# Optimization experiments

Measured on AMD Instinct MI355X. Metric: run time of the kernel, lower is better.

The kernel has to match this reference:

```python
import jax, jax.numpy as jnp
import numpy as np

N, E, B, P = 50000, 800000, 64, 3
F_E = F_N = F_G = 16
D, H = 64, 128  # embedding/target dim, hidden dim
NEG_SLOPE = 0.01


def _lrelu(z):
    return jax.nn.leaky_relu(z, NEG_SLOPE)


def _mlp3(z, w1, b1, w2, b2, w3, b3):
    z = _lrelu(z @ w1 + b1)
    z = _lrelu(z @ w2 + b2)
    return z @ w3 + b3


def setup_inputs() -> dict:
    key = jax.random.key(0)
    ks = iter(jax.random.split(key, 64))
    s = 0.05

    def lin(i, o, stack=None):
        shp = (i, o) if stack is None else (stack, i, o)
        return jax.random.normal(next(ks), shp, jnp.float32) * s

    def bias(o, stack=None):
        shp = (o,) if stack is None else (stack, o)
        return jax.random.normal(next(ks), shp, jnp.float32) * s

    inp = {}
    inp['x'] = jax.random.normal(next(ks), (N, F_N), jnp.float32)
    inp['edge_attr'] = jax.random.normal(next(ks), (E, F_E), jnp.float32)
    inp['u'] = jax.random.normal(next(ks), (B, F_G), jnp.float32)
    # embeddings
    inp['emb_e_w'], inp['emb_e_b'] = lin(F_E, D), bias(D)
    inp['emb_n_w'], inp['emb_n_b'] = lin(F_N, D), bias(D)
    inp['emb_g_w'], inp['emb_g_b'] = lin(F_G, D), bias(D)
    # message-passing params, stacked over P passes (dims identical since emb==target)
    inp['ew1'], inp['eb1'] = lin(4 * D, H, P), bias(H, P)   # src,dest,edge,global -> 256
    inp['ew2'], inp['eb2'] = lin(H, H, P), bias(H, P)
    inp['ew3'], inp['eb3'] = lin(H, D, P), bias(D, P)
    inp['nw1'], inp['nb1'] = lin(3 * D, H, P), bias(H, P)   # node,edge_agg,global -> 192
    inp['nw2'], inp['nb2'] = lin(H, H, P), bias(H, P)
    inp['nw3'], inp['nb3'] = lin(H, D, P), bias(D, P)
    inp['gw1'], inp['gb1'] = lin(2 * D, H, P), bias(H, P)   # global,node_agg -> 128
    inp['gw2'], inp['gb2'] = lin(H, H, P), bias(H, P)
    inp['gw3'], inp['gb3'] = lin(H, D, P), bias(D, P)
    # decoders
    inp['dec_w'], inp['dec_b'] = lin(D, 1), bias(1)
    inp['vw1'], inp['vb1'] = lin(D, D), bias(D)
    inp['vw2'], inp['vb2'] = lin(D, 1), bias(1)
    # graph structure
    inp['edge_index'] = jax.random.randint(next(ks), (2, E), 0, N, jnp.int32)
    inp['batch'] = jnp.sort(jax.random.randint(next(ks), (N,), 0, B, jnp.int32))
    return inp


def reference(x, edge_attr, u,
              emb_e_w, emb_e_b, emb_n_w, emb_n_b, emb_g_w, emb_g_b,
              ew1, eb1, ew2, eb2, ew3, eb3,
              nw1, nb1, nw2, nb2, nw3, nb3,
              gw1, gb1, gw2, gb2, gw3, gb3,
              dec_w, dec_b, vw1, vb1, vw2, vb2,
              edge_index, batch):
    n_nodes, n_graphs = x.shape[0], u.shape[0]
    row, col = edge_index[0], edge_index[1]

    # embeddings
    e = _lrelu(edge_attr @ emb_e_w + emb_e_b)   # [E, D]
    xh = _lrelu(x @ emb_n_w + emb_n_b)          # [N, D]
    g = _lrelu(u @ emb_g_w + emb_g_b)           # [B, D]

    for p in range(ew1.shape[0]):
        # EdgeModel: gather src/dest/global, MLP
        e_in = jnp.concatenate([xh[row], xh[col], e, g[batch[row]]], axis=1)
        e_new = _mlp3(e_in, ew1[p], eb1[p], ew2[p], eb2[p], ew3[p], eb3[p])
        # NodeModel: scatter_add NEW edge features to dest nodes
        e_agg = jax.ops.segment_sum(e_new, col, num_segments=n_nodes)
        n_in = jnp.concatenate([xh, e_agg, g[batch]], axis=1)
        x_new = _mlp3(n_in, nw1[p], nb1[p], nw2[p], nb2[p], nw3[p], nb3[p])
        # GlobalModel: scatter_add NEW node features per graph
        x_agg = jax.ops.segment_sum(x_new, batch, num_segments=n_graphs)
        g_in = jnp.concatenate([g, x_agg], axis=1)
        g_new = _mlp3(g_in, gw1[p], gb1[p], gw2[p], gb2[p], gw3[p], gb3[p])
        # residual updates
        xh, e, g = xh + x_new, e + e_new, g + g_new

    edge_out = e @ dec_w + dec_b                      # [E, 1]
    value_out = _lrelu(g @ vw1 + vb1) @ vw2 + vb2     # [B, 1]
    return edge_out, value_out
```

## Files before the change

kernel.cpp:

```cpp
#include <hip/hip_runtime.h>
#include <hip/hip_bf16.h>
#include <stdint.h>

typedef unsigned short u16;
typedef unsigned int u32;
typedef short s16x8 __attribute__((ext_vector_type(8)));
typedef float f32x4 __attribute__((ext_vector_type(4)));

#define NN 50000
#define EE 800000
#define BB 64
#define PP 3

__device__ __forceinline__ float b2f(u16 x){ union{u32 u; float f;} c; c.u=((u32)x)<<16; return c.f; }
__device__ __forceinline__ u16 f2b(float v){ union{float f; u32 u;} c; c.f=v; u32 u=c.u; return (u16)((u + 0x7fffu + ((u>>16)&1u))>>16); }
__device__ __forceinline__ float lrelu(float v){ return v>0.f ? v : 0.01f*v; }
__device__ __forceinline__ f32x4 MFMA(s16x8 a, s16x8 b, f32x4 c){
  return __builtin_amdgcn_mfma_f32_16x16x32_bf16(a,b,c,0,0,0);
}

__device__ __forceinline__ int xcd_swz(int bid, int nwg){
  int q = nwg>>3, r = nwg&7;
  int x = bid&7, i = bid>>3;
  return (x<r ? x*(q+1) : r*(q+1)+(x-r)*q) + i;
}

__global__ __launch_bounds__(256) void k_hist(const int* __restrict__ eidx, int* __restrict__ hist){
  int e = blockIdx.x*256 + threadIdx.x;
  if (e < EE) atomicAdd(&hist[eidx[EE+e]], 1);
}

__global__ __launch_bounds__(1024) void k_scan(const int* __restrict__ hist, int* __restrict__ offs){
  __shared__ int lsums[1024];
  const int tid = threadIdx.x;
  const int CH = 49;
  int base = tid*CH;
  int s = 0;
  for (int i=0;i<CH;i++){ int b=base+i; if (b<NN) s += hist[b]; }
  lsums[tid]=s; __syncthreads();
  for (int off=1; off<1024; off<<=1){
    int v = (tid>=off)? lsums[tid-off] : 0;
    __syncthreads();
    lsums[tid] += v;
    __syncthreads();
  }
  int run = (tid>0)? lsums[tid-1] : 0;
  for (int i=0;i<CH;i++){ int b=base+i; if (b<NN){ offs[b]=run; run+=hist[b]; } }
}

__global__ __launch_bounds__(256) void k_scatter(const int* __restrict__ eidx, int* __restrict__ offs,
                                                 int* __restrict__ perm, int* __restrict__ dcols,
                                                 int* __restrict__ inv){
  int e = blockIdx.x*256 + threadIdx.x;
  if (e >= EE) return;
  int col = eidx[EE+e];
  int pos = atomicAdd(&offs[col], 1);
  perm[pos] = e;
  dcols[pos] = col;
  inv[e] = pos;
}

__global__ __launch_bounds__(256) void k_repack(const float* __restrict__ W, u16* __restrict__ out, int K, int Nn){
  int chunks_pp = (K/32)*(Nn/16)*64;
  int t = blockIdx.x*256 + threadIdx.x;
  if (t >= PP*chunks_pp) return;
  int p = t/chunks_pp, rem = t%chunks_pp;
  int NB = Nn/16;
  int kb = rem/(NB*64); int r2 = rem%(NB*64);
  int nb = r2/64; int l = r2&63;
  const float* Wp = W + (size_t)p*K*Nn;
  int k0 = kb*32 + ((l>>4)<<3), n = nb*16 + (l&15);
  u16 tmp[8];
  #pragma unroll
  for (int j=0;j<8;j++) tmp[j] = f2b(Wp[(size_t)(k0+j)*Nn + n]);
  *(uint4*)(out + (size_t)t*8) = *(uint4*)tmp;
}

template<bool SCATTER>
__global__ __launch_bounds__(256) void k_embed(const float* __restrict__ in, const float* __restrict__ W,
                                               const float* __restrict__ b, u16* __restrict__ out, int nrows,
                                               const int* __restrict__ inv){
  __shared__ float wl[1024];
  __shared__ float bl[64];
  int tid = threadIdx.x;
  for (int i=tid;i<1024;i+=256) wl[i]=W[i];
  if (tid<64) bl[tid]=b[tid];
  __syncthreads();
  int row = blockIdx.x*256 + tid;
  if (row >= nrows) return;
  float inb[16];
  const float4* src4=(const float4*)(in + (size_t)row*16);
  #pragma unroll
  for (int q=0;q<4;q++){ float4 v=src4[q]; inb[q*4]=v.x; inb[q*4+1]=v.y; inb[q*4+2]=v.z; inb[q*4+3]=v.w; }
  float acc[64];
  #pragma unroll
  for (int j=0;j<64;j++) acc[j]=bl[j];
  #pragma unroll
  for (int k=0;k<16;k++){
    float a = inb[k];
    const float4* wr4 = (const float4*)(wl + k*64);
    #pragma unroll
    for (int j4=0;j4<16;j4++){
      float4 w4 = wr4[j4];
      acc[j4*4+0] += a*w4.x; acc[j4*4+1] += a*w4.y;
      acc[j4*4+2] += a*w4.z; acc[j4*4+3] += a*w4.w;
    }
  }
  u16 ob[64];
  #pragma unroll
  for (int j=0;j<64;j++) ob[j]=f2b(lrelu(acc[j]));
  int drow = SCATTER ? inv[row] : row;
  uint4* dst=(uint4*)(out + (size_t)drow*64);
  #pragma unroll
  for (int j=0;j<8;j++) dst[j]=((uint4*)ob)[j];
}

__global__ void k_embed_g(const float* __restrict__ in, const float* __restrict__ W, const float* __restrict__ b,
                          u16* __restrict__ g_b, float* __restrict__ g_f){
  __shared__ float wl[1024];
  __shared__ float bl[64];
  int tid = threadIdx.x;
  for (int i=tid;i<1024;i+=64) wl[i]=W[i];
  if (tid<64) bl[tid]=b[tid];
  __syncthreads();
  int row = tid;
  float inb[16];
  const float4* src4=(const float4*)(in + (size_t)row*16);
  #pragma unroll
  for (int q=0;q<4;q++){ float4 v=src4[q]; inb[q*4]=v.x; inb[q*4+1]=v.y; inb[q*4+2]=v.z; inb[q*4+3]=v.w; }
  float acc[64];
  #pragma unroll
  for (int j=0;j<64;j++) acc[j]=bl[j];
  #pragma unroll
  for (int k=0;k<16;k++){
    float a = inb[k];
    const float* wr = wl + k*64;
    #pragma unroll
    for (int j=0;j<64;j++) acc[j] += a*wr[j];
  }
  #pragma unroll
  for (int j=0;j<64;j++){
    float v = lrelu(acc[j]);
    g_f[row*64+j] = v;
    g_b[row*64+j] = f2b(v);
  }
}

__device__ __forceinline__ void rmw16(u16* p, const float* vals){
  uint4 q0=((uint4*)p)[0], q1=((uint4*)p)[1];
  const u16* h0=(const u16*)&q0; const u16* hq=(const u16*)&q1;
  u16 o[16];
  #pragma unroll
  for (int c=0;c<8;c++) o[c]=f2b(b2f(h0[c])+vals[c]);
  #pragma unroll
  for (int c=0;c<8;c++) o[8+c]=f2b(b2f(hq[c])+vals[8+c]);
  ((uint4*)p)[0]=*(uint4*)o; ((uint4*)p)[1]=*(uint4*)(o+8);
}

template<int K0, int MODE, bool LAST>
__global__ __launch_bounds__(256,4) void k_mlp(
    u16* __restrict__ xh_b, u16* __restrict__ e_b,
    float* __restrict__ eagg, float* __restrict__ xagg,
    u16* __restrict__ g_b, float* __restrict__ g_f,
    const int* __restrict__ eidx, const int* __restrict__ batch,
    const int* __restrict__ perm, const int* __restrict__ dcols,
    const uint4* __restrict__ w1f, const uint4* __restrict__ w2f, const uint4* __restrict__ w3f,
    const float* __restrict__ b1, const float* __restrict__ b2, const float* __restrict__ b3,
    const float* __restrict__ dw, const float* __restrict__ db, float* __restrict__ outp)
{
  constexpr int KB  = K0/32;
  constexpr int RS  = K0*2;
  constexpr int A0SZ = (64*RS > 32768) ? 64*RS : 32768;
  __shared__ __align__(16) char a0[A0SZ];
  __shared__ int s_edge[64];
  __shared__ int s_dcol[64];
  char* h1 = a0;
  char* h2 = a0 + 16384;
  char* h3 = a0;

  const int tid  = threadIdx.x;
  const int wave = tid>>6, lane = tid&63;
  const int rowbase = (MODE==2 ? blockIdx.x : xcd_swz(blockIdx.x, gridDim.x))*64;
  const int lrow = lane&15;
  const int lsw  = (lane&7)<<4;
  const int aoff = (lane>>4)*16;
  const int qc   = (lane>>4)*4;

  s16x8 wA[KB][2];
  #pragma unroll
  for (int kb=0;kb<KB;kb++){
    #pragma unroll
    for (int j=0;j<2;j++)
      wA[kb][j] = *(const s16x8*)(w1f + (size_t)(kb*8 + wave*2 + j)*64 + lane);
  }

  {
    const int r = tid>>2, s = tid&3;
    char* drow = a0 + r*RS;
    const int sw = (r&7)<<4;
    if (MODE==0){
      const int slot = rowbase + r;
      const int edge = perm[slot];
      if (s==0){ s_edge[r]=edge; s_dcol[r]=dcols[slot]; }
      const int er = eidx[edge], ec = eidx[EE+edge];
      const u16* src = (s==0)? xh_b + (size_t)er*64
                     : (s==1)? xh_b + (size_t)ec*64
                     : (s==2)? e_b  + (size_t)slot*64
                     :         g_b  + (size_t)batch[er]*64;
      const uint4* s4=(const uint4*)src;
      #pragma unroll
      for (int j=0;j<8;j++)
        *(uint4*)(drow + ((s*128 + j*16) ^ sw)) = s4[j];
    } else if (MODE==1){
      const int node = rowbase + r;
      const bool ok = node < NN;
      if (s==0){
        const uint4* s4=(const uint4*)(xh_b + (size_t)node*64);
        #pragma unroll
        for (int j=0;j<8;j++){ uint4 v={0,0,0,0}; if (ok) v=s4[j];
          *(uint4*)(drow + ((j*16) ^ sw)) = v; }
      } else if (s==1){
        const float4* s4=(const float4*)(eagg + (size_t)node*64);
        #pragma unroll
        for (int j=0;j<8;j++){
          u16 tmp[8]={0,0,0,0,0,0,0,0};
          if (ok){ float4 lo=s4[2*j], hi=s4[2*j+1];
            tmp[0]=f2b(lo.x);tmp[1]=f2b(lo.y);tmp[2]=f2b(lo.z);tmp[3]=f2b(lo.w);
            tmp[4]=f2b(hi.x);tmp[5]=f2b(hi.y);tmp[6]=f2b(hi.z);tmp[7]=f2b(hi.w); }
          *(uint4*)(drow + ((128 + j*16) ^ sw)) = *(uint4*)tmp;
        }
      } else if (s==2){
        int bidx = ok ? batch[node] : 0;
        const uint4* s4=(const uint4*)(g_b + (size_t)bidx*64);
        #pragma unroll
        for (int j=0;j<8;j++){ uint4 v={0,0,0,0}; if (ok) v=s4[j];
          *(uint4*)(drow + ((256 + j*16) ^ sw)) = v; }
      }
    } else {
      if (s==0){
        const uint4* s4=(const uint4*)(g_b + (size_t)r*64);
        #pragma unroll
        for (int j=0;j<8;j++) *(uint4*)(drow + ((j*16) ^ sw)) = s4[j];
      } else if (s==1){
        const float4* s4=(const float4*)(xagg + (size_t)r*64);
        #pragma unroll
        for (int j=0;j<8;j++){
          u16 tmp[8];
          float4 lo=s4[2*j], hi=s4[2*j+1];
          tmp[0]=f2b(lo.x);tmp[1]=f2b(lo.y);tmp[2]=f2b(lo.z);tmp[3]=f2b(lo.w);
          tmp[4]=f2b(hi.x);tmp[5]=f2b(hi.y);tmp[6]=f2b(hi.z);tmp[7]=f2b(hi.w);
          *(uint4*)(drow + ((128 + j*16) ^ sw)) = *(uint4*)tmp;
        }
      }
    }
  }
  __syncthreads();

  f32x4 acc[4][2];
  #pragma unroll
  for (int rb=0;rb<4;rb++){ acc[rb][0]=f32x4{0,0,0,0}; acc[rb][1]=f32x4{0,0,0,0}; }
  #pragma unroll
  for (int kb=0;kb<KB;kb++){
    #pragma unroll
    for (int rb=0;rb<4;rb++){
      s16x8 af = *(const s16x8*)(a0 + (rb*16+lrow)*RS + ((kb*64 + aoff) ^ lsw));
      acc[rb][0] = MFMA(wA[kb][0], af, acc[rb][0]);
      acc[rb][1] = MFMA(wA[kb][1], af, acc[rb][1]);
    }
  }

  s16x8 wB[4][2];
  #pragma unroll
  for (int kb=0;kb<4;kb++){
    #pragma unroll
    for (int j=0;j<2;j++)
      wB[kb][j] = *(const s16x8*)(w2f + (size_t)(kb*8 + wave*2 + j)*64 + lane);
  }
  __syncthreads();

  #pragma unroll
  for (int j=0;j<2;j++){
    const float4 bs = *(const float4*)(b1 + wave*32 + j*16 + qc);
    #pragma unroll
    for (int rb=0;rb<4;rb++){
      int row = rb*16 + lrow;
      int c2 = (wave*32 + j*16 + qc)*2;
      u16 t0=f2b(lrelu(acc[rb][j][0]+bs.x)), t1=f2b(lrelu(acc[rb][j][1]+bs.y));
      u16 t2=f2b(lrelu(acc[rb][j][2]+bs.z)), t3=f2b(lrelu(acc[rb][j][3]+bs.w));
      uint2 pk = make_uint2((u32)t0 | ((u32)t1<<16), (u32)t2 | ((u32)t3<<16));
      *(uint2*)(h1 + row*256 + (c2 ^ ((row&7)<<4))) = pk;
    }
  }
  __syncthreads();

  f32x4 acc2[4][2];
  #pragma unroll
  for (int rb=0;rb<4;rb++){ acc2[rb][0]=f32x4{0,0,0,0}; acc2[rb][1]=f32x4{0,0,0,0}; }
  #pragma unroll
  for (int kb=0;kb<4;kb++){
    #pragma unroll
    for (int rb=0;rb<4;rb++){
      s16x8 af = *(const s16x8*)(h1 + (rb*16+lrow)*256 + ((kb*64 + aoff) ^ lsw));
      acc2[rb][0] = MFMA(wB[kb][0], af, acc2[rb][0]);
      acc2[rb][1] = MFMA(wB[kb][1], af, acc2[rb][1]);
    }
  }

  s16x8 wC[4];
  #pragma unroll
  for (int kb=0;kb<4;kb++)
    wC[kb] = *(const s16x8*)(w3f + (size_t)(kb*4 + wave)*64 + lane);

  #pragma unroll
  for (int j=0;j<2;j++){
    const float4 bs = *(const float4*)(b2 + wave*32 + j*16 + qc);
    #pragma unroll
    for (int rb=0;rb<4;rb++){
      int row = rb*16 + lrow;
      int c2 = (wave*32 + j*16 + qc)*2;
      u16 t0=f2b(lrelu(acc2[rb][j][0]+bs.x)), t1=f2b(lrelu(acc2[rb][j][1]+bs.y));
      u16 t2=f2b(lrelu(acc2[rb][j][2]+bs.z)), t3=f2b(lrelu(acc2[rb][j][3]+bs.w));
      uint2 pk = make_uint2((u32)t0 | ((u32)t1<<16), (u32)t2 | ((u32)t3<<16));
      *(uint2*)(h2 + row*256 + (c2 ^ ((row&7)<<4))) = pk;
    }
  }
  __syncthreads();

  f32x4 acc3[4];
  #pragma unroll
  for (int rb=0;rb<4;rb++) acc3[rb]=f32x4{0,0,0,0};
  #pragma unroll
  for (int kb=0;kb<4;kb++){
    #pragma unroll
    for (int rb=0;rb<4;rb++){
      s16x8 af = *(const s16x8*)(h2 + (rb*16+lrow)*256 + ((kb*64 + aoff) ^ lsw));
      acc3[rb] = MFMA(wC[kb], af, acc3[rb]);
    }
  }
  {
    const float4 b3v = *(const float4*)(b3 + wave*16 + qc);
    #pragma unroll
    for (int rb=0;rb<4;rb++){
      int row = rb*16 + lrow;
      int c4 = (wave*16 + qc)*4;
      float4 o = make_float4(acc3[rb][0]+b3v.x, acc3[rb][1]+b3v.y, acc3[rb][2]+b3v.z, acc3[rb][3]+b3v.w);
      *(float4*)(h3 + row*256 + (c4 ^ ((row&7)<<4))) = o;
    }
  }
  __syncthreads();

  const int r2 = tid>>2, cs = (tid&3)*16;
  const int rsw2 = (r2&7)<<4;
  if (MODE==0){
    const int slot = rowbase + r2;
    float vals[16];
    #pragma unroll
    for (int c=0;c<16;c++) vals[c]=*(const float*)(h3 + r2*256 + (((cs+c)*4)^rsw2));
    if (LAST){
      const int edge = s_edge[r2];
      u16* p = e_b + (size_t)slot*64 + cs;
      uint4 q0=((uint4*)p)[0], q1=((uint4*)p)[1];
      const u16* h0=(const u16*)&q0; const u16* hq=(const u16*)&q1;
      float dwl[16];
      const float4* dw4 = (const float4*)(dw + cs);
      #pragma unroll
      for (int q=0;q<4;q++){ float4 v=dw4[q]; dwl[q*4]=v.x; dwl[q*4+1]=v.y; dwl[q*4+2]=v.z; dwl[q*4+3]=v.w; }
      u16 o[16]; float part=0.f;
      #pragma unroll
      for (int c=0;c<8;c++){ u16 nb16=f2b(b2f(h0[c])+vals[c]); o[c]=nb16; part += b2f(nb16)*dwl[c]; }
      #pragma unroll
      for (int c=0;c<8;c++){ u16 nb16=f2b(b2f(hq[c])+vals[8+c]); o[8+c]=nb16; part += b2f(nb16)*dwl[8+c]; }
      ((uint4*)p)[0]=*(uint4*)o; ((uint4*)p)[1]=*(uint4*)(o+8);
      part += __shfl_xor(part,1);
      part += __shfl_xor(part,2);
      if ((tid&3)==0) outp[edge] = part + db[0];
    } else {
      rmw16(e_b + (size_t)slot*64 + cs, vals);
    }
    const int col64 = tid&63, rg = tid>>6;
    float ssum = 0.f; int cur = -1;
    #pragma unroll
    for (int rr=0;rr<16;rr++){
      int row = rg*16+rr;
      int gid = s_dcol[row];
      float v = *(const float*)(h3 + row*256 + ((col64*4) ^ ((row&7)<<4)));
      if (gid != cur){ if (cur>=0) unsafeAtomicAdd(eagg + (size_t)cur*64 + col64, ssum); ssum=0.f; cur=gid; }
      ssum += v;
    }
    if (cur>=0) unsafeAtomicAdd(eagg + (size_t)cur*64 + col64, ssum);
  } else if (MODE==1){
    const int node = rowbase + r2;
    if (node < NN){
      float vals[16];
      #pragma unroll
      for (int c=0;c<16;c++) vals[c]=*(const float*)(h3 + r2*256 + (((cs+c)*4)^rsw2));
      rmw16(xh_b + (size_t)node*64 + cs, vals);
    }
    const int col = tid&63, rg = tid>>6;
    float s = 0.f; int cur = -1;
    for (int rr=0;rr<16;rr++){
      int row = rg*16+rr; int nd = rowbase+row;
      int gid = (nd<NN) ? batch[nd] : -1;
      float v = *(const float*)(h3 + row*256 + ((col*4) ^ ((row&7)<<4)));
      if (gid != cur){ if (cur>=0) unsafeAtomicAdd(xagg + cur*64 + col, s); s=0.f; cur=gid; }
      if (gid>=0) s += v;
    }
    if (cur>=0) unsafeAtomicAdd(xagg + cur*64 + col, s);
  } else {
    float vals[16];
    #pragma unroll
    for (int c=0;c<16;c++) vals[c]=*(const float*)(h3 + r2*256 + (((cs+c)*4)^rsw2));
    #pragma unroll
    for (int c=0;c<16;c++){
      int idx = r2*64 + cs + c;
      float nv = g_f[idx] + vals[c];
      g_f[idx] = nv; g_b[idx] = f2b(nv);
    }
  }
}

__global__ void k_value(const float* __restrict__ g_f, const float* __restrict__ vw1, const float* __restrict__ vb1,
                        const float* __restrict__ vw2, const float* __restrict__ vb2, float* __restrict__ out){
  __shared__ float w1[4096];
  __shared__ float b1s[64];
  __shared__ float w2[64];
  int tid=threadIdx.x;
  for (int i=tid;i<4096;i+=64) w1[i]=vw1[i];
  if (tid<64){ b1s[tid]=vb1[tid]; w2[tid]=vw2[tid]; }
  __syncthreads();
  float gi[64];
  #pragma unroll
  for (int k=0;k<64;k++) gi[k]=g_f[tid*64+k];
  float val=vb2[0];
  for (int j=0;j<64;j++){
    float s=b1s[j];
    #pragma unroll
    for (int k=0;k<64;k++) s+=gi[k]*w1[k*64+j];
    val += lrelu(s)*w2[j];
  }
  out[tid]=val;
}

extern "C" void kernel_launch(void* const* d_in, const int* in_sizes, int n_in,
                              void* d_out, int out_size, void* d_ws, size_t ws_size,
                              hipStream_t stream){
  const float* x    =(const float*)d_in[0];
  const float* ea   =(const float*)d_in[1];
  const float* uu   =(const float*)d_in[2];
  const float* eew  =(const float*)d_in[3];
  const float* eeb  =(const float*)d_in[4];
  const float* enw  =(const float*)d_in[5];
  const float* enb  =(const float*)d_in[6];
  const float* egw  =(const float*)d_in[7];
  const float* egb  =(const float*)d_in[8];
  const float* ew1  =(const float*)d_in[9];
  const float* eb1  =(const float*)d_in[10];
  const float* ew2  =(const float*)d_in[11];
  const float* eb2  =(const float*)d_in[12];
  const float* ew3  =(const float*)d_in[13];
  const float* eb3  =(const float*)d_in[14];
  const float* nw1  =(const float*)d_in[15];
  const float* nb1  =(const float*)d_in[16];
  const float* nw2  =(const float*)d_in[17];
  const float* nb2  =(const float*)d_in[18];
  const float* nw3  =(const float*)d_in[19];
  const float* nb3  =(const float*)d_in[20];
  const float* gw1  =(const float*)d_in[21];
  const float* gb1  =(const float*)d_in[22];
  const float* gw2  =(const float*)d_in[23];
  const float* gb2  =(const float*)d_in[24];
  const float* gw3  =(const float*)d_in[25];
  const float* gb3  =(const float*)d_in[26];
  const float* dw   =(const float*)d_in[27];
  const float* db   =(const float*)d_in[28];
  const float* vw1  =(const float*)d_in[29];
  const float* vb1  =(const float*)d_in[30];
  const float* vw2  =(const float*)d_in[31];
  const float* vb2  =(const float*)d_in[32];
  const int* eidx =(const int*)d_in[33];
  const int* batch=(const int*)d_in[34];

  char* ws=(char*)d_ws; size_t off=0;
  auto alloc=[&](size_t b)->char*{ char* p=ws+off; off=(off+b+255)&~(size_t)255; return p; };
  u16*   xh_b =(u16*)  alloc((size_t)NN*64*2);
  u16*   e_s  =(u16*)  alloc((size_t)EE*64*2);
  float* eagg =(float*)alloc((size_t)NN*64*4);
  float* xagg =(float*)alloc((size_t)BB*64*4);
  u16*   g_bb =(u16*)  alloc((size_t)BB*64*2);
  float* g_f  =(float*)alloc((size_t)BB*64*4);
  u16* ew1f=(u16*)alloc((size_t)PP*4096*16);
  u16* ew2f=(u16*)alloc((size_t)PP*2048*16);
  u16* ew3f=(u16*)alloc((size_t)PP*1024*16);
  u16* nw1f=(u16*)alloc((size_t)PP*3072*16);
  u16* nw2f=(u16*)alloc((size_t)PP*2048*16);
  u16* nw3f=(u16*)alloc((size_t)PP*1024*16);
  u16* gw1f=(u16*)alloc((size_t)PP*2048*16);
  u16* gw2f=(u16*)alloc((size_t)PP*2048*16);
  u16* gw3f=(u16*)alloc((size_t)PP*1024*16);
  int* hist =(int*)alloc((size_t)NN*4);
  int* offs =(int*)alloc((size_t)NN*4);
  int* perm =(int*)alloc((size_t)EE*4);
  int* dcols=(int*)alloc((size_t)EE*4);
  int* inv  =(int*)alloc((size_t)EE*4);
  float* out=(float*)d_out;

  hipMemsetAsync(hist, 0, (size_t)NN*4, stream);
  k_hist<<<(EE+255)/256,256,0,stream>>>(eidx, hist);
  k_scan<<<1,1024,0,stream>>>(hist, offs);
  k_scatter<<<(EE+255)/256,256,0,stream>>>(eidx, offs, perm, dcols, inv);

  auto rp=[&](const float* W, u16* dst, int K, int Nn){
    int total = PP*(K/32)*(Nn/16)*64;
    k_repack<<<(total+255)/256,256,0,stream>>>(W,dst,K,Nn);
  };
  rp(ew1,ew1f,256,128); rp(ew2,ew2f,128,128); rp(ew3,ew3f,128,64);
  rp(nw1,nw1f,192,128); rp(nw2,nw2f,128,128); rp(nw3,nw3f,128,64);
  rp(gw1,gw1f,128,128); rp(gw2,gw2f,128,128); rp(gw3,gw3f,128,64);

  k_embed<true ><<<(EE+255)/256,256,0,stream>>>(ea, eew, eeb, e_s, EE, inv);
  k_embed<false><<<(NN+255)/256,256,0,stream>>>(x,  enw, enb, xh_b, NN, nullptr);
  k_embed_g<<<1,64,0,stream>>>(uu, egw, egb, g_bb, g_f);

  for (int p=0;p<PP;p++){
    hipMemsetAsync(eagg, 0, (size_t)NN*64*4, stream);
    hipMemsetAsync(xagg, 0, (size_t)BB*64*4, stream);
    if (p<PP-1)
      k_mlp<256,0,false><<<EE/64,256,0,stream>>>(xh_b,e_s,eagg,xagg,g_bb,g_f,eidx,batch,perm,dcols,
          (const uint4*)ew1f + (size_t)p*4096, (const uint4*)ew2f + (size_t)p*2048, (const uint4*)ew3f + (size_t)p*1024,
          eb1+p*128, eb2+p*128, eb3+p*64, dw, db, out);
    else
      k_mlp<256,0,true><<<EE/64,256,0,stream>>>(xh_b,e_s,eagg,xagg,g_bb,g_f,eidx,batch,perm,dcols,
          (const uint4*)ew1f + (size_t)p*4096, (const uint4*)ew2f + (size_t)p*2048, (const uint4*)ew3f + (size_t)p*1024,
          eb1+p*128, eb2+p*128, eb3+p*64, dw, db, out);
    k_mlp<192,1,false><<<(NN+63)/64,256,0,stream>>>(xh_b,e_s,eagg,xagg,g_bb,g_f,eidx,batch,perm,dcols,
        (const uint4*)nw1f + (size_t)p*3072, (const uint4*)nw2f + (size_t)p*2048, (const uint4*)nw3f + (size_t)p*1024,
        nb1+p*128, nb2+p*128, nb3+p*64, dw, db, out);
    k_mlp<128,2,false><<<1,256,0,stream>>>(xh_b,e_s,eagg,xagg,g_bb,g_f,eidx,batch,perm,dcols,
        (const uint4*)gw1f + (size_t)p*2048, (const uint4*)gw2f + (size_t)p*2048, (const uint4*)gw3f + (size_t)p*1024,
        gb1+p*128, gb2+p*128, gb3+p*64, dw, db, out);
  }
  k_value<<<1,64,0,stream>>>(g_f, vw1, vb1, vw2, vb2, out+EE);
}
```

Before: 1.160 ms.

## Precompute sorted src/batch indices and keep residual inputs in registers

The scatter kernel now also writes the source node and graph id for each sorted edge slot. The edge MLP can then fetch all gather indices directly instead of chasing perm→eidx→batch. The gather is restructured so each of the four threads per row loads a 32-byte slice of every input segment rather than one whole segment. The old edge/node features are held in registers and reused for the residual update, removing the global re-read in the epilogue. Launch bounds are raised to 5 blocks/SM and LDS index arrays replaced by register-preloaded ids, at the cost of extra register pressure and two more E-sized index arrays.

```diff
diff --git a/kernel.cpp b/kernel.cpp
--- a/kernel.cpp
+++ b/kernel.cpp
@@ -50,14 +50,18 @@
 
 __global__ __launch_bounds__(256) void k_scatter(const int* __restrict__ eidx, int* __restrict__ offs,
                                                  int* __restrict__ perm, int* __restrict__ dcols,
-                                                 int* __restrict__ inv){
+                                                 int* __restrict__ inv, int* __restrict__ rows_s,
+                                                 int* __restrict__ gbs, const int* __restrict__ batch){
   int e = blockIdx.x*256 + threadIdx.x;
   if (e >= EE) return;
   int col = eidx[EE+e];
+  int er  = eidx[e];
   int pos = atomicAdd(&offs[col], 1);
   perm[pos] = e;
   dcols[pos] = col;
   inv[e] = pos;
+  rows_s[pos] = er;
+  gbs[pos] = batch[er];
 }
 
 __global__ __launch_bounds__(256) void k_repack(const float* __restrict__ W, u16* __restrict__ out, int K, int Nn){
@@ -146,34 +150,21 @@
   }
 }
 
-__device__ __forceinline__ void rmw16(u16* p, const float* vals){
-  uint4 q0=((uint4*)p)[0], q1=((uint4*)p)[1];
-  const u16* h0=(const u16*)&q0; const u16* hq=(const u16*)&q1;
-  u16 o[16];
-  #pragma unroll
-  for (int c=0;c<8;c++) o[c]=f2b(b2f(h0[c])+vals[c]);
-  #pragma unroll
-  for (int c=0;c<8;c++) o[8+c]=f2b(b2f(hq[c])+vals[8+c]);
-  ((uint4*)p)[0]=*(uint4*)o; ((uint4*)p)[1]=*(uint4*)(o+8);
-}
-
 template<int K0, int MODE, bool LAST>
-__global__ __launch_bounds__(256,4) void k_mlp(
+__global__ __launch_bounds__(256,5) void k_mlp(
     u16* __restrict__ xh_b, u16* __restrict__ e_b,
     float* __restrict__ eagg, float* __restrict__ xagg,
     u16* __restrict__ g_b, float* __restrict__ g_f,
-    const int* __restrict__ eidx, const int* __restrict__ batch,
+    const int* __restrict__ batch,
     const int* __restrict__ perm, const int* __restrict__ dcols,
+    const int* __restrict__ rows_s, const int* __restrict__ gbs,
     const uint4* __restrict__ w1f, const uint4* __restrict__ w2f, const uint4* __restrict__ w3f,
     const float* __restrict__ b1, const float* __restrict__ b2, const float* __restrict__ b3,
     const float* __restrict__ dw, const float* __restrict__ db, float* __restrict__ outp)
 {
   constexpr int KB  = K0/32;
   constexpr int RS  = K0*2;
-  constexpr int A0SZ = (64*RS > 32768) ? 64*RS : 32768;
-  __shared__ __align__(16) char a0[A0SZ];
-  __shared__ int s_edge[64];
-  __shared__ int s_dcol[64];
+  __shared__ __align__(16) char a0[32768];
   char* h1 = a0;
   char* h2 = a0 + 16384;
   char* h3 = a0;
@@ -186,6 +177,8 @@
   const int aoff = (lane>>4)*16;
   const int qc   = (lane>>4)*4;
 
+  uint4 old0 = {0,0,0,0}, old1 = {0,0,0,0};
+
   s16x8 wA[KB][2];
   #pragma unroll
   for (int kb=0;kb<KB;kb++){
@@ -198,60 +191,57 @@
     const int r = tid>>2, s = tid&3;
     char* drow = a0 + r*RS;
     const int sw = (r&7)<<4;
+    const int base = s*32;
     if (MODE==0){
       const int slot = rowbase + r;
-      const int edge = perm[slot];
-      if (s==0){ s_edge[r]=edge; s_dcol[r]=dcols[slot]; }
-      const int er = eidx[edge], ec = eidx[EE+edge];
-      const u16* src = (s==0)? xh_b + (size_t)er*64
-                     : (s==1)? xh_b + (size_t)ec*64
-                     : (s==2)? e_b  + (size_t)slot*64
-                     :         g_b  + (size_t)batch[er]*64;
-      const uint4* s4=(const uint4*)src;
-      #pragma unroll
-      for (int j=0;j<8;j++)
-        *(uint4*)(drow + ((s*128 + j*16) ^ sw)) = s4[j];
+      const int er = rows_s[slot];
+      const int ec = dcols[slot];
+      const int gb = gbs[slot];
+      const uint4* p0=(const uint4*)(xh_b + (size_t)er*64 + s*16);
+      const uint4* p1=(const uint4*)(xh_b + (size_t)ec*64 + s*16);
+      const uint4* p2=(const uint4*)(e_b  + (size_t)slot*64 + s*16);
+      const uint4* p3=(const uint4*)(g_b  + (size_t)gb*64 + s*16);
+      uint4 a_=p0[0], b_=p0[1], c_=p1[0], d_=p1[1];
+      old0=p2[0]; old1=p2[1];
+      uint4 g0=p3[0], g1=p3[1];
+      *(uint4*)(drow + ((  0+base   ) ^ sw)) = a_;   *(uint4*)(drow + ((  0+base+16) ^ sw)) = b_;
+      *(uint4*)(drow + ((128+base   ) ^ sw)) = c_;   *(uint4*)(drow + ((128+base+16) ^ sw)) = d_;
+      *(uint4*)(drow + ((256+base   ) ^ sw)) = old0; *(uint4*)(drow + ((256+base+16) ^ sw)) = old1;
+      *(uint4*)(drow + ((384+base   ) ^ sw)) = g0;   *(uint4*)(drow + ((384+base+16) ^ sw)) = g1;
     } else if (MODE==1){
       const int node = rowbase + r;
       const bool ok = node < NN;
-      if (s==0){
-        const uint4* s4=(const uint4*)(xh_b + (size_t)node*64);
-        #pragma unroll
-        for (int j=0;j<8;j++){ uint4 v={0,0,0,0}; if (ok) v=s4[j];
-          *(uint4*)(drow + ((j*16) ^ sw)) = v; }
-      } else if (s==1){
-        const float4* s4=(const float4*)(eagg + (size_t)node*64);
-        #pragma unroll
-        for (int j=0;j<8;j++){
-          u16 tmp[8]={0,0,0,0,0,0,0,0};
-          if (ok){ float4 lo=s4[2*j], hi=s4[2*j+1];
-            tmp[0]=f2b(lo.x);tmp[1]=f2b(lo.y);tmp[2]=f2b(lo.z);tmp[3]=f2b(lo.w);
-            tmp[4]=f2b(hi.x);tmp[5]=f2b(hi.y);tmp[6]=f2b(hi.z);tmp[7]=f2b(hi.w); }
-          *(uint4*)(drow + ((128 + j*16) ^ sw)) = *(uint4*)tmp;
-        }
-      } else if (s==2){
-        int bidx = ok ? batch[node] : 0;
-        const uint4* s4=(const uint4*)(g_b + (size_t)bidx*64);
-        #pragma unroll
-        for (int j=0;j<8;j++){ uint4 v={0,0,0,0}; if (ok) v=s4[j];
-          *(uint4*)(drow + ((256 + j*16) ^ sw)) = v; }
+      uint4 z={0,0,0,0};
+      uint4 g0=z, g1=z;
+      u16 t[16]={0,0,0,0,0,0,0,0,0,0,0,0,0,0,0,0};
+      if (ok){
+        const uint4* p0=(const uint4*)(xh_b + (size_t)node*64 + s*16);
+        old0=p0[0]; old1=p0[1];
+        const float4* p1=(const float4*)(eagg + (size_t)node*64 + s*16);
+        float4 f0=p1[0], f1=p1[1], f2v=p1[2], f3=p1[3];
+        t[0]=f2b(f0.x); t[1]=f2b(f0.y); t[2]=f2b(f0.z); t[3]=f2b(f0.w);
+        t[4]=f2b(f1.x); t[5]=f2b(f1.y); t[6]=f2b(f1.z); t[7]=f2b(f1.w);
+        t[8]=f2b(f2v.x); t[9]=f2b(f2v.y); t[10]=f2b(f2v.z); t[11]=f2b(f2v.w);
+        t[12]=f2b(f3.x); t[13]=f2b(f3.y); t[14]=f2b(f3.z); t[15]=f2b(f3.w);
+        const int bidx = batch[node];
+        const uint4* p2=(const uint4*)(g_b + (size_t)bidx*64 + s*16);
+        g0=p2[0]; g1=p2[1];
       }
+      *(uint4*)(drow + ((  0+base   ) ^ sw)) = ok?old0:z; *(uint4*)(drow + ((  0+base+16) ^ sw)) = ok?old1:z;
+      *(uint4*)(drow + ((128+base   ) ^ sw)) = ((uint4*)t)[0]; *(uint4*)(drow + ((128+base+16) ^ sw)) = ((uint4*)t)[1];
+      *(uint4*)(drow + ((256+base   ) ^ sw)) = g0; *(uint4*)(drow + ((256+base+16) ^ sw)) = g1;
     } else {
-      if (s==0){
-        const uint4* s4=(const uint4*)(g_b + (size_t)r*64);
-        #pragma unroll
-        for (int j=0;j<8;j++) *(uint4*)(drow + ((j*16) ^ sw)) = s4[j];
-      } else if (s==1){
-        const float4* s4=(const float4*)(xagg + (size_t)r*64);
-        #pragma unroll
-        for (int j=0;j<8;j++){
-          u16 tmp[8];
-          float4 lo=s4[2*j], hi=s4[2*j+1];
-          tmp[0]=f2b(lo.x);tmp[1]=f2b(lo.y);tmp[2]=f2b(lo.z);tmp[3]=f2b(lo.w);
-          tmp[4]=f2b(hi.x);tmp[5]=f2b(hi.y);tmp[6]=f2b(hi.z);tmp[7]=f2b(hi.w);
-          *(uint4*)(drow + ((128 + j*16) ^ sw)) = *(uint4*)tmp;
-        }
-      }
+      const uint4* p0=(const uint4*)(g_b + (size_t)r*64 + s*16);
+      uint4 a_=p0[0], b_=p0[1];
+      const float4* p1=(const float4*)(xagg + (size_t)r*64 + s*16);
+      float4 f0=p1[0], f1=p1[1], f2v=p1[2], f3=p1[3];
+      u16 t[16];
+      t[0]=f2b(f0.x); t[1]=f2b(f0.y); t[2]=f2b(f0.z); t[3]=f2b(f0.w);
+      t[4]=f2b(f1.x); t[5]=f2b(f1.y); t[6]=f2b(f1.z); t[7]=f2b(f1.w);
+      t[8]=f2b(f2v.x); t[9]=f2b(f2v.y); t[10]=f2b(f2v.z); t[11]=f2b(f2v.w);
+      t[12]=f2b(f3.x); t[13]=f2b(f3.y); t[14]=f2b(f3.z); t[15]=f2b(f3.w);
+      *(uint4*)(drow + ((  0+base   ) ^ sw)) = a_; *(uint4*)(drow + ((  0+base+16) ^ sw)) = b_;
+      *(uint4*)(drow + ((128+base   ) ^ sw)) = ((uint4*)t)[0]; *(uint4*)(drow + ((128+base+16) ^ sw)) = ((uint4*)t)[1];
     }
   }
   __syncthreads();
@@ -356,33 +346,36 @@
     float vals[16];
     #pragma unroll
     for (int c=0;c<16;c++) vals[c]=*(const float*)(h3 + r2*256 + (((cs+c)*4)^rsw2));
+    const u16* eo0=(const u16*)&old0; const u16* eo1=(const u16*)&old1;
+    u16 o[16];
+    #pragma unroll
+    for (int c=0;c<8;c++) o[c]   = f2b(b2f(eo0[c]) + vals[c]);
+    #pragma unroll
+    for (int c=0;c<8;c++) o[8+c] = f2b(b2f(eo1[c]) + vals[8+c]);
+    u16* p = e_b + (size_t)slot*64 + cs;
+    ((uint4*)p)[0]=((uint4*)o)[0]; ((uint4*)p)[1]=((uint4*)o)[1];
     if (LAST){
-      const int edge = s_edge[r2];
-      u16* p = e_b + (size_t)slot*64 + cs;
-      uint4 q0=((uint4*)p)[0], q1=((uint4*)p)[1];
-      const u16* h0=(const u16*)&q0; const u16* hq=(const u16*)&q1;
+      const int edge = perm[slot];
       float dwl[16];
       const float4* dw4 = (const float4*)(dw + cs);
       #pragma unroll
       for (int q=0;q<4;q++){ float4 v=dw4[q]; dwl[q*4]=v.x; dwl[q*4+1]=v.y; dwl[q*4+2]=v.z; dwl[q*4+3]=v.w; }
-      u16 o[16]; float part=0.f;
+      float part=0.f;
       #pragma unroll
-      for (int c=0;c<8;c++){ u16 nb16=f2b(b2f(h0[c])+vals[c]); o[c]=nb16; part += b2f(nb16)*dwl[c]; }
-      #pragma unroll
-      for (int c=0;c<8;c++){ u16 nb16=f2b(b2f(hq[c])+vals[8+c]); o[8+c]=nb16; part += b2f(nb16)*dwl[8+c]; }
-      ((uint4*)p)[0]=*(uint4*)o; ((uint4*)p)[1]=*(uint4*)(o+8);
+      for (int c=0;c<16;c++) part += b2f(o[c])*dwl[c];
       part += __shfl_xor(part,1);
       part += __shfl_xor(part,2);
       if ((tid&3)==0) outp[edge] = part + db[0];
-    } else {
-      rmw16(e_b + (size_t)slot*64 + cs, vals);
     }
     const int col64 = tid&63, rg = tid>>6;
+    int gids[16];
+    #pragma unroll
+    for (int rr=0;rr<16;rr++) gids[rr] = dcols[rowbase + rg*16 + rr];
     float ssum = 0.f; int cur = -1;
     #pragma unroll
     for (int rr=0;rr<16;rr++){
       int row = rg*16+rr;
-      int gid = s_dcol[row];
+      int gid = gids[rr];
       float v = *(const float*)(h3 + row*256 + ((col64*4) ^ ((row&7)<<4)));
       if (gid != cur){ if (cur>=0) unsafeAtomicAdd(eagg + (size_t)cur*64 + col64, ssum); ssum=0.f; cur=gid; }
       ssum += v;
@@ -394,13 +387,24 @@
       float vals[16];
       #pragma unroll
       for (int c=0;c<16;c++) vals[c]=*(const float*)(h3 + r2*256 + (((cs+c)*4)^rsw2));
-      rmw16(xh_b + (size_t)node*64 + cs, vals);
+      const u16* xo0=(const u16*)&old0; const u16* xo1=(const u16*)&old1;
+      u16 o[16];
+      #pragma unroll
+      for (int c=0;c<8;c++) o[c]   = f2b(b2f(xo0[c]) + vals[c]);
+      #pragma unroll
+      for (int c=0;c<8;c++) o[8+c] = f2b(b2f(xo1[c]) + vals[8+c]);
+      u16* p = xh_b + (size_t)node*64 + cs;
+      ((uint4*)p)[0]=((uint4*)o)[0]; ((uint4*)p)[1]=((uint4*)o)[1];
     }
     const int col = tid&63, rg = tid>>6;
+    int gids[16];
+    #pragma unroll
+    for (int rr=0;rr<16;rr++){ int nd=rowbase+rg*16+rr; gids[rr] = (nd<NN)? batch[nd] : -1; }
     float s = 0.f; int cur = -1;
+    #pragma unroll
     for (int rr=0;rr<16;rr++){
-      int row = rg*16+rr; int nd = rowbase+row;
-      int gid = (nd<NN) ? batch[nd] : -1;
+      int row = rg*16+rr;
+      int gid = gids[rr];
       float v = *(const float*)(h3 + row*256 + ((col*4) ^ ((row&7)<<4)));
       if (gid != cur){ if (cur>=0) unsafeAtomicAdd(xagg + cur*64 + col, s); s=0.f; cur=gid; }
       if (gid>=0) s += v;
@@ -497,17 +501,19 @@
   u16* gw1f=(u16*)alloc((size_t)PP*2048*16);
   u16* gw2f=(u16*)alloc((size_t)PP*2048*16);
   u16* gw3f=(u16*)alloc((size_t)PP*1024*16);
-  int* hist =(int*)alloc((size_t)NN*4);
-  int* offs =(int*)alloc((size_t)NN*4);
-  int* perm =(int*)alloc((size_t)EE*4);
-  int* dcols=(int*)alloc((size_t)EE*4);
-  int* inv  =(int*)alloc((size_t)EE*4);
+  int* hist  =(int*)alloc((size_t)NN*4);
+  int* offs  =(int*)alloc((size_t)NN*4);
+  int* perm  =(int*)alloc((size_t)EE*4);
+  int* dcols =(int*)alloc((size_t)EE*4);
+  int* inv   =(int*)alloc((size_t)EE*4);
+  int* rows_s=(int*)alloc((size_t)EE*4);
+  int* gbs   =(int*)alloc((size_t)EE*4);
   float* out=(float*)d_out;
 
   hipMemsetAsync(hist, 0, (size_t)NN*4, stream);
   k_hist<<<(EE+255)/256,256,0,stream>>>(eidx, hist);
   k_scan<<<1,1024,0,stream>>>(hist, offs);
-  k_scatter<<<(EE+255)/256,256,0,stream>>>(eidx, offs, perm, dcols, inv);
+  k_scatter<<<(EE+255)/256,256,0,stream>>>(eidx, offs, perm, dcols, inv, rows_s, gbs, batch);
 
   auto rp=[&](const float* W, u16* dst, int K, int Nn){
     int total = PP*(K/32)*(Nn/16)*64;
@@ -525,17 +531,17 @@
     hipMemsetAsync(eagg, 0, (size_t)NN*64*4, stream);
     hipMemsetAsync(xagg, 0, (size_t)BB*64*4, stream);
     if (p<PP-1)
-      k_mlp<256,0,false><<<EE/64,256,0,stream>>>(xh_b,e_s,eagg,xagg,g_bb,g_f,eidx,batch,perm,dcols,
+      k_mlp<256,0,false><<<EE/64,256,0,stream>>>(xh_b,e_s,eagg,xagg,g_bb,g_f,batch,perm,dcols,rows_s,gbs,
           (const uint4*)ew1f + (size_t)p*4096, (const uint4*)ew2f + (size_t)p*2048, (const uint4*)ew3f + (size_t)p*1024,
           eb1+p*128, eb2+p*128, eb3+p*64, dw, db, out);
     else
-      k_mlp<256,0,true><<<EE/64,256,0,stream>>>(xh_b,e_s,eagg,xagg,g_bb,g_f,eidx,batch,perm,dcols,
+      k_mlp<256,0,true><<<EE/64,256,0,stream>>>(xh_b,e_s,eagg,xagg,g_bb,g_f,batch,perm,dcols,rows_s,gbs,
           (const uint4*)ew1f + (size_t)p*4096, (const uint4*)ew2f + (size_t)p*2048, (const uint4*)ew3f + (size_t)p*1024,
           eb1+p*128, eb2+p*128, eb3+p*64, dw, db, out);
-    k_mlp<192,1,false><<<(NN+63)/64,256,0,stream>>>(xh_b,e_s,eagg,xagg,g_bb,g_f,eidx,batch,perm,dcols,
+    k_mlp<192,1,false><<<(NN+63)/64,256,0,stream>>>(xh_b,e_s,eagg,xagg,g_bb,g_f,batch,perm,dcols,rows_s,gbs,
         (const uint4*)nw1f + (size_t)p*3072, (const uint4*)nw2f + (size_t)p*2048, (const uint4*)nw3f + (size_t)p*1024,
         nb1+p*128, nb2+p*128, nb3+p*64, dw, db, out);
-    k_mlp<128,2,false><<<1,256,0,stream>>>(xh_b,e_s,eagg,xagg,g_bb,g_f,eidx,batch,perm,dcols,
+    k_mlp<128,2,false><<<1,256,0,stream>>>(xh_b,e_s,eagg,xagg,g_bb,g_f,batch,perm,dcols,rows_s,gbs,
         (const uint4*)gw1f + (size_t)p*2048, (const uint4*)gw2f + (size_t)p*2048, (const uint4*)gw3f + (size_t)p*1024,
         gb1+p*128, gb2+p*128, gb3+p*64, dw, db, out);
   }
```

Result: faster. 1.113 ms (-4.1%).
